# Performance work log

Measured on AMD Instinct MI355X. Metric: run time of the kernel, lower is better.

## Reference

```python
import jax, jax.numpy as jnp
import numpy as np

B, S, D = 2, 2048, 2048
H = 16
DR = 64      # qk_rope_head_dim
DN = 64      # qk_nope_head_dim
DQK = DN + DR
DV = 128     # v_head_dim
QLR = 1536   # q_lora_rank
KVLR = 1024  # kv_lora_rank
THETA = 10000.0


def setup_inputs() -> dict:
    key = jax.random.key(0)
    ks = jax.random.split(key, 8)
    init = lambda k, shape: (jax.random.normal(k, shape, jnp.float32) * 0.02)
    x = jax.random.normal(ks[0], (B, S, D), jnp.float32)
    wq_a = init(ks[1], (QLR, D))
    q_norm_w = jnp.ones((QLR,), jnp.float32)
    wq_b = init(ks[2], (H * DQK, QLR))
    wkv_a = init(ks[3], (KVLR + DR, D))
    kv_norm_w = jnp.ones((KVLR,), jnp.float32)
    wkv_b = init(ks[4], (H * (DN + DV), KVLR))
    wo = init(ks[5], (D, H * DV))
    # rotary frequencies: angle[t, i] = t / theta^(2i/DR)  (complex freqs_cis = cos + i sin)
    inv_freq = 1.0 / (THETA ** (jnp.arange(0, DR, 2, dtype=jnp.float32) / DR))
    ang = jnp.arange(S, dtype=jnp.float32)[:, None] * inv_freq[None, :]  # [S, DR/2]
    freqs_cos, freqs_sin = jnp.cos(ang), jnp.sin(ang)
    # causal additive mask (large negative instead of -inf for grad safety)
    mask = jnp.where(jnp.triu(jnp.ones((S, S), bool), 1), -1e9, 0.0).astype(jnp.float32)
    return dict(x=x, wq_a=wq_a, q_norm_w=q_norm_w, wq_b=wq_b, wkv_a=wkv_a,
                kv_norm_w=kv_norm_w, wkv_b=wkv_b, wo=wo, mask=mask,
                freqs_cos=freqs_cos, freqs_sin=freqs_sin, start_pos=0)


def _rmsnorm(x, w, eps=1e-6):
    return x * jax.lax.rsqrt(jnp.mean(x * x, axis=-1, keepdims=True) + eps) * w


def _rope(x, cos, sin):
    # x: [B, S, h, d]; complex multiply on interleaved (even, odd) pairs
    x0, x1 = x[..., ::2], x[..., 1::2]
    c = cos[None, :, None, :]
    s = sin[None, :, None, :]
    return jnp.stack([x0 * c - x1 * s, x0 * s + x1 * c], axis=-1).reshape(x.shape)


def reference(x, wq_a, q_norm_w, wq_b, wkv_a, kv_norm_w, wkv_b, wo,
              mask, freqs_cos, freqs_sin, start_pos):
    # start_pos == 0 prefill: KV cache[:end_pos] equals current K/V.
    scale = DQK ** -0.5
    # low-rank Q: wq_b(q_norm(wq_a(x)))
    q = _rmsnorm(x @ wq_a.T, q_norm_w) @ wq_b.T
    q = q.reshape(B, S, H, DQK)
    q_nope, q_pe = q[..., :DN], q[..., DN:]
    q_pe = _rope(q_pe, freqs_cos, freqs_sin)
    # latent KV
    kv = x @ wkv_a.T                              # [B, S, KVLR + DR]
    c_kv, k_pe = kv[..., :KVLR], kv[..., KVLR:]
    k_pe = _rope(k_pe[:, :, None, :], freqs_cos, freqs_sin)   # [B, S, 1, DR]
    kv2 = (_rmsnorm(c_kv, kv_norm_w) @ wkv_b.T).reshape(B, S, H, DN + DV)
    k_nope, v = kv2[..., :DN], kv2[..., DN:]
    k = jnp.concatenate([k_nope, jnp.broadcast_to(k_pe, (B, S, H, DR))], axis=-1)
    qf = jnp.concatenate([q_nope, q_pe], axis=-1)             # [B, S, H, DQK]
    # scores laid out [B, S(q), H, T(k)] as in the torch code
    scores = jnp.einsum('bshd,bthd->bsht', qf, k) * scale + mask[None, :, None, :]
    attn = jax.nn.softmax(scores.astype(jnp.float32), axis=-1).astype(x.dtype)
    out = jnp.einsum('bsht,bthd->bshd', attn, v)              # [B, S, H, DV]
    return out.reshape(B, S, H * DV) @ wo.T
```

## Files before the change

### kernel.cpp

```cpp
#include <hip/hip_runtime.h>
#include <hip/hip_bf16.h>


using bf16 = __hip_bfloat16;
typedef __attribute__((ext_vector_type(8))) short bf16x8;
typedef __attribute__((ext_vector_type(4))) float f32x4;

#define S_ 2048
#define NEG_BIG (-1e30f)
#define LOG2E 1.4426950408889634f

static __device__ __forceinline__ f32x4 mfma16(bf16x8 a, bf16x8 b, f32x4 c) {
    return __builtin_amdgcn_mfma_f32_16x16x32_bf16(a, b, c, 0, 0, 0);
}

static __device__ __forceinline__ void gload_lds16(const bf16* g, bf16* l) {
    __builtin_amdgcn_global_load_lds(
        (const __attribute__((address_space(1))) void*)g,
        (__attribute__((address_space(3))) void*)l, 16, 0, 0);
}

__global__ __launch_bounds__(256) void f2b(const float* __restrict__ src,
                                           bf16* __restrict__ dst, int n4) {
    int i = blockIdx.x * 256 + threadIdx.x;
    if (i < n4) {
        float4 v = ((const float4*)src)[i];
        alignas(8) bf16 t[4];
        t[0] = (bf16)v.x; t[1] = (bf16)v.y; t[2] = (bf16)v.z; t[3] = (bf16)v.w;
        ((uint2*)dst)[i] = *(const uint2*)t;
    }
}

template <bool C_F32>
__global__ __launch_bounds__(256) void gemm_bt(const bf16* __restrict__ A,
                                               const bf16* __restrict__ Bw,
                                               void* __restrict__ Cv,
                                               int M, int N, int K,
                                               int lda, int ldb, int ldc) {
    __shared__ bf16 As[2][128 * 32];
    __shared__ bf16 Bs[2][128 * 32];
    const int tid = threadIdx.x;
    int bx = blockIdx.x, by = blockIdx.y;
    {
        int nwg = gridDim.x * gridDim.y;
        if ((nwg & 7) == 0) {
            int wg = by * gridDim.x + bx;
            int swz = (wg & 7) * (nwg >> 3) + (wg >> 3);
            bx = swz % gridDim.x;
            by = swz / gridDim.x;
        }
    }
    const int m0 = bx * 128;
    const int n0 = by * 128;
    const int w = tid >> 6, lane = tid & 63, quad = lane >> 4, l15 = lane & 15;
    const int wr = (w >> 1) * 64, wc = (w & 1) * 64;

    f32x4 acc[4][4];
#pragma unroll
    for (int i = 0; i < 4; i++)
#pragma unroll
        for (int j = 0; j < 4; j++) acc[i][j] = (f32x4){0.f, 0.f, 0.f, 0.f};

    auto stage = [&](int buf, int k0) {
#pragma unroll
        for (int cc = 0; cc < 2; cc++) {
            int c = tid + cc * 256;
            int row = c >> 2;
            int chunk = (c & 3) ^ ((row >> 1) & 3);
            gload_lds16(A + (size_t)(m0 + row) * lda + k0 + chunk * 8, &As[buf][c * 8]);
            gload_lds16(Bw + (size_t)(n0 + row) * ldb + k0 + chunk * 8, &Bs[buf][c * 8]);
        }
    };

    stage(0, 0);
    __syncthreads();
    int cur = 0;
    for (int k0 = 0; k0 < K; k0 += 32) {
        if (k0 + 32 < K) stage(cur ^ 1, k0 + 32);
        const bf16* Asc = As[cur];
        const bf16* Bsc = Bs[cur];
        bf16x8 af[4], bfr[4];
#pragma unroll
        for (int mi = 0; mi < 4; mi++) {
            int row = wr + mi * 16 + l15;
            int chunkE = quad ^ ((row >> 1) & 3);
            af[mi] = *(const bf16x8*)(&Asc[row * 32 + chunkE * 8]);
        }
#pragma unroll
        for (int ni = 0; ni < 4; ni++) {
            int row = wc + ni * 16 + l15;
            int chunkE = quad ^ ((row >> 1) & 3);
            bfr[ni] = *(const bf16x8*)(&Bsc[row * 32 + chunkE * 8]);
        }
#pragma unroll
        for (int mi = 0; mi < 4; mi++)
#pragma unroll
            for (int ni = 0; ni < 4; ni++)
                acc[mi][ni] = mfma16(af[mi], bfr[ni], acc[mi][ni]);
        __syncthreads();
        cur ^= 1;
    }

#pragma unroll
    for (int mi = 0; mi < 4; mi++) {
#pragma unroll
        for (int ni = 0; ni < 4; ni++) {
            int col = n0 + wc + ni * 16 + l15;
            if (col < N) {
#pragma unroll
                for (int r = 0; r < 4; r++) {
                    int row = m0 + wr + mi * 16 + quad * 4 + r;
                    if (C_F32) ((float*)Cv)[(size_t)row * ldc + col] = acc[mi][ni][r];
                    else       ((bf16*)Cv)[(size_t)row * ldc + col] = (bf16)acc[mi][ni][r];
                }
            }
        }
    }
}

__global__ void rmsnorm_ip(bf16* __restrict__ buf, const float* __restrict__ w,
                           int cols, int ld) {
    int row = blockIdx.x;
    bf16* p = buf + (size_t)row * ld;
    float ss = 0.f;
    for (int c = threadIdx.x; c < cols; c += 256) {
        float v = __bfloat162float(p[c]);
        ss += v * v;
    }
#pragma unroll
    for (int off = 32; off; off >>= 1) ss += __shfl_down(ss, off, 64);
    __shared__ float red[4];
    __shared__ float rnorm_s;
    if ((threadIdx.x & 63) == 0) red[threadIdx.x >> 6] = ss;
    __syncthreads();
    if (threadIdx.x == 0)
        rnorm_s = rsqrtf((red[0] + red[1] + red[2] + red[3]) / cols + 1e-6f);
    __syncthreads();
    float rn = rnorm_s;
    for (int c = threadIdx.x; c < cols; c += 256) {
        float v = __bfloat162float(p[c]);
        p[c] = (bf16)(v * rn * w[c]);
    }
}

__global__ void rope_k(const bf16* __restrict__ cq, bf16* __restrict__ kpe,
                       const float* __restrict__ fc, const float* __restrict__ fs) {
    int id = blockIdx.x * 256 + threadIdx.x;
    int row = id >> 5, i = id & 31;
    int s = row & (S_ - 1);
    const bf16* p = cq + (size_t)row * 2624 + 1024 + 2 * i;
    float x0 = __bfloat162float(p[0]), x1 = __bfloat162float(p[1]);
    float c = fc[s * 32 + i], sn = fs[s * 32 + i];
    bf16* q = kpe + (size_t)row * 64 + 2 * i;
    q[0] = (bf16)(x0 * c - x1 * sn);
    q[1] = (bf16)(x0 * sn + x1 * c);
}

__global__ void rope_q(bf16* __restrict__ qb, const float* __restrict__ fc,
                       const float* __restrict__ fs) {
    int id = blockIdx.x * 256 + threadIdx.x;
    int row = id >> 9, rest = id & 511, h = rest >> 5, i = rest & 31;
    int s = row & (S_ - 1);
    bf16* p = qb + (size_t)row * 2048 + h * 128 + 64 + 2 * i;
    float x0 = __bfloat162float(p[0]), x1 = __bfloat162float(p[1]);
    float c = fc[s * 32 + i], sn = fs[s * 32 + i];
    p[0] = (bf16)(x0 * c - x1 * sn);
    p[1] = (bf16)(x0 * sn + x1 * c);
}

__global__ __launch_bounds__(512) void attn_kernel(const bf16* __restrict__ Qg,
                                                   const bf16* __restrict__ KV2,
                                                   const bf16* __restrict__ KPE,
                                                   bf16* __restrict__ Og) {
    __shared__ bf16 Ks[64 * 128];
    __shared__ bf16 Vt[128 * 64];
    const int tid = threadIdx.x;
    const int h = blockIdx.y;
    const int b = blockIdx.z;
    const int w = tid >> 6, lane = tid & 63, quad = lane >> 4, l15 = lane & 15;
    const int grp = w >> 2, wl = w & 3;
    const int jB = 31 - (int)blockIdx.x;
    const int q0 = (grp ? jB : (int)blockIdx.x) * 64;
    const int qrow = q0 + wl * 16 + l15;
    const float scl2 = 0.08838834764831845f * LOG2E;

    bf16x8 qf[4];
    {
        const bf16* qp = Qg + ((size_t)(b * S_) + qrow) * 2048 + h * 128 + quad * 8;
#pragma unroll
        for (int kk = 0; kk < 4; kk++) qf[kk] = *(const bf16x8*)(qp + kk * 32);
    }

    f32x4 acc_o[8];
#pragma unroll
    for (int j = 0; j < 8; j++) acc_o[j] = (f32x4){0.f, 0.f, 0.f, 0.f};
    float m_i = NEG_BIG, l_i = 0.f;
    const int s_base = q0 + wl * 16 + quad * 4;
    const int tend = jB * 64;

    const int dv0 = (tid >> 4) * 4;
    const int tv0 = (tid & 15) * 4;

    for (int t0 = 0; t0 <= tend; t0 += 64) {
        __syncthreads();
#pragma unroll
        for (int cc = 0; cc < 2; cc++) {
            int c = tid + cc * 512;
            int trow = c >> 4, chunk = c & 15;
            int col8 = chunk * 8;
            size_t grow = (size_t)(b * S_) + t0 + trow;
            int4 v;
            if (col8 < 64) v = *(const int4*)(KV2 + grow * 3072 + h * 192 + col8);
            else           v = *(const int4*)(KPE + grow * 64 + col8 - 64);
            int chunkE = chunk ^ (trow & 7);
            *(int4*)(&Ks[trow * 128 + chunkE * 8]) = v;
        }
        {
            size_t grow0 = (size_t)(b * S_) + t0 + tv0;
            alignas(16) bf16 va[4][4];
#pragma unroll
            for (int i = 0; i < 4; i++)
                *(uint2*)va[i] = *(const uint2*)(KV2 + (grow0 + i) * 3072 + h * 192 + 64 + dv0);
#pragma unroll
            for (int j = 0; j < 4; j++) {
                alignas(8) bf16 tmp[4] = {va[0][j], va[1][j], va[2][j], va[3][j]};
                int dv = dv0 + j;
                int cE = (tv0 >> 3) ^ (dv & 7);
                *(uint2*)(&Vt[dv * 64 + cE * 8 + (tv0 & 7)]) = *(uint2*)tmp;
            }
        }
        __syncthreads();
        if (t0 > q0) continue;

        f32x4 sc[4];
#pragma unroll
        for (int ni = 0; ni < 4; ni++) sc[ni] = (f32x4){0.f, 0.f, 0.f, 0.f};
#pragma unroll
        for (int kk = 0; kk < 4; kk++) {
#pragma unroll
            for (int ni = 0; ni < 4; ni++) {
                int trow = ni * 16 + l15;
                int chunkE = (kk * 4 + quad) ^ (trow & 7);
                bf16x8 kf = *(const bf16x8*)(&Ks[trow * 128 + chunkE * 8]);
                sc[ni] = mfma16(kf, qf[kk], sc[ni]);
            }
        }
        float xv[4][4];
        float pmax = NEG_BIG;
#pragma unroll
        for (int ni = 0; ni < 4; ni++) {
#pragma unroll
            for (int r = 0; r < 4; r++) {
                int t = t0 + ni * 16 + quad * 4 + r;
                float x = sc[ni][r] * scl2;
                if (t > qrow) x = NEG_BIG;
                xv[ni][r] = x;
                pmax = fmaxf(pmax, x);
            }
        }
        pmax = fmaxf(pmax, __shfl_xor(pmax, 16, 64));
        pmax = fmaxf(pmax, __shfl_xor(pmax, 32, 64));
        if (!__all(pmax - m_i <= 8.0f)) {
            float mn = fmaxf(m_i, pmax);
            float alpha = exp2f(m_i - mn);
            m_i = mn;
            l_i *= alpha;
            float ar[4];
#pragma unroll
            for (int r = 0; r < 4; r++) ar[r] = __shfl(alpha, quad * 4 + r, 64);
#pragma unroll
            for (int nj = 0; nj < 8; nj++)
#pragma unroll
                for (int r = 0; r < 4; r++) acc_o[nj][r] *= ar[r];
        }
        float rsum = 0.f;
#pragma unroll
        for (int ni = 0; ni < 4; ni++)
#pragma unroll
            for (int r = 0; r < 4; r++) {
                float e = exp2f(xv[ni][r] - m_i);
                xv[ni][r] = e;
                rsum += e;
            }
        rsum += __shfl_xor(rsum, 16, 64);
        rsum += __shfl_xor(rsum, 32, 64);
        l_i += rsum;

#pragma unroll
        for (int sg = 0; sg < 2; sg++) {
            alignas(16) bf16 pfa[8];
#pragma unroll
            for (int j = 0; j < 4; j++) {
                pfa[j]     = (bf16)xv[2 * sg][j];
                pfa[j + 4] = (bf16)xv[2 * sg + 1][j];
            }
            bf16x8 pf = *(const bf16x8*)pfa;
            const int cLo = sg * 4 + (quad >> 1);
            const int cHi = cLo + 2;
            const int off = (quad & 1) * 4;
#pragma unroll
            for (int nj = 0; nj < 8; nj++) {
                int dv = nj * 16 + l15;
                int d7 = dv & 7;
                alignas(16) bf16 vfa[8];
                *(uint2*)&vfa[0] = *(const uint2*)&Vt[dv * 64 + ((cLo ^ d7) * 8) + off];
                *(uint2*)&vfa[4] = *(const uint2*)&Vt[dv * 64 + ((cHi ^ d7) * 8) + off];
                bf16x8 vf = *(const bf16x8*)vfa;
                acc_o[nj] = mfma16(pf, vf, acc_o[nj]);
            }
        }
    }
    float lr[4];
#pragma unroll
    for (int r = 0; r < 4; r++) lr[r] = __shfl(l_i, quad * 4 + r, 64);
#pragma unroll
    for (int nj = 0; nj < 8; nj++) {
        int col = h * 128 + nj * 16 + l15;
#pragma unroll
        for (int r = 0; r < 4; r++) {
            float v = acc_o[nj][r] / lr[r];
            Og[((size_t)(b * S_) + s_base + r) * 2048 + col] = (bf16)v;
        }
    }
}

extern "C" void kernel_launch(void* const* d_in, const int* in_sizes, int n_in,
                              void* d_out, int out_size, void* d_ws, size_t ws_size,
                              hipStream_t stream) {
    const float* x        = (const float*)d_in[0];
    const float* wq_a     = (const float*)d_in[1];
    const float* q_norm_w = (const float*)d_in[2];
    const float* wq_b     = (const float*)d_in[3];
    const float* wkv_a    = (const float*)d_in[4];
    const float* kv_norm_w= (const float*)d_in[5];
    const float* wkv_b    = (const float*)d_in[6];
    const float* wo       = (const float*)d_in[7];
    const float* fcos     = (const float*)d_in[9];
    const float* fsin     = (const float*)d_in[10];
    float* out = (float*)d_out;

    char* ws = (char*)d_ws;
    bf16* kv2   = (bf16*)(ws);
    bf16* kpe   = (bf16*)(ws + 25165824);
    bf16* cq    = (bf16*)(ws + 25690112);
    bf16* xb    = (bf16*)(ws + 47185920);
    bf16* wslot = (bf16*)(ws + 63963136);
    bf16* attno = cq;
    bf16* qbuf  = (bf16*)d_out;

    dim3 blk(256);
    f2b<<<8192, blk, 0, stream>>>(x, xb, 2097152);
    f2b<<<2176, blk, 0, stream>>>(wkv_a, wslot, 557056);
    f2b<<<3072, blk, 0, stream>>>(wq_a, wslot + 1088 * 2048, 786432);
    gemm_bt<false><<<dim3(32, 21), blk, 0, stream>>>(xb, wslot, cq, 4096, 2624, 2048, 2048, 2048, 2624);
    rope_k<<<512, blk, 0, stream>>>(cq, kpe, fcos, fsin);
    rmsnorm_ip<<<4096, blk, 0, stream>>>(cq, kv_norm_w, 1024, 2624);
    f2b<<<3072, blk, 0, stream>>>(wkv_b, wslot, 786432);
    gemm_bt<false><<<dim3(32, 24), blk, 0, stream>>>(cq, wslot, kv2, 4096, 3072, 1024, 2624, 1024, 3072);
    rmsnorm_ip<<<4096, blk, 0, stream>>>(cq + 1088, q_norm_w, 1536, 2624);
    f2b<<<3072, blk, 0, stream>>>(wq_b, wslot, 786432);
    gemm_bt<false><<<dim3(32, 16), blk, 0, stream>>>(cq + 1088, wslot, qbuf, 4096, 2048, 1536, 2624, 1536, 2048);
    rope_q<<<8192, blk, 0, stream>>>(qbuf, fcos, fsin);
    attn_kernel<<<dim3(16, 16, 2), dim3(512), 0, stream>>>(qbuf, kv2, kpe, attno);
    f2b<<<4096, blk, 0, stream>>>(wo, wslot, 1048576);
    gemm_bt<true><<<dim3(32, 16), blk, 0, stream>>>(attno, wslot, out, 4096, 2048, 2048, 2048, 2048, 2048);
}
```

Measured before the change: 482.0 us.

## Split attention KV range into two halves with a separate combine kernel

The causal attention kernel now runs twice as many blocks. Each block covers either the lower or upper half of the key tiles for its paired query tiles and writes unnormalized-then-normalized partial outputs plus per-row (max, sum) statistics. A new combine kernel rescales and merges the two partial outputs before the output projection, aiming to raise parallelism and CU occupancy. This costs extra global traffic for the partial buffers and one more launch. Separately, the GEMM drops its workgroup index swizzle, which may change L2 reuse.

```diff
diff --git a/kernel.cpp b/kernel.cpp
--- a/kernel.cpp
+++ b/kernel.cpp
@@ -40,18 +40,8 @@
     __shared__ bf16 As[2][128 * 32];
     __shared__ bf16 Bs[2][128 * 32];
     const int tid = threadIdx.x;
-    int bx = blockIdx.x, by = blockIdx.y;
-    {
-        int nwg = gridDim.x * gridDim.y;
-        if ((nwg & 7) == 0) {
-            int wg = by * gridDim.x + bx;
-            int swz = (wg & 7) * (nwg >> 3) + (wg >> 3);
-            bx = swz % gridDim.x;
-            by = swz / gridDim.x;
-        }
-    }
-    const int m0 = bx * 128;
-    const int n0 = by * 128;
+    const int m0 = blockIdx.x * 128;
+    const int n0 = blockIdx.y * 128;
     const int w = tid >> 6, lane = tid & 63, quad = lane >> 4, l15 = lane & 15;
     const int wr = (w >> 1) * 64, wc = (w & 1) * 64;
 
@@ -171,12 +161,15 @@
 __global__ __launch_bounds__(512) void attn_kernel(const bf16* __restrict__ Qg,
                                                    const bf16* __restrict__ KV2,
                                                    const bf16* __restrict__ KPE,
-                                                   bf16* __restrict__ Og) {
+                                                   bf16* __restrict__ pO0,
+                                                   bf16* __restrict__ pO1,
+                                                   float2* __restrict__ ml) {
     __shared__ bf16 Ks[64 * 128];
     __shared__ bf16 Vt[128 * 64];
     const int tid = threadIdx.x;
     const int h = blockIdx.y;
-    const int b = blockIdx.z;
+    const int zz = blockIdx.z;
+    const int b = zz >> 1, half = zz & 1;
     const int w = tid >> 6, lane = tid & 63, quad = lane >> 4, l15 = lane & 15;
     const int grp = w >> 2, wl = w & 3;
     const int jB = 31 - (int)blockIdx.x;
@@ -184,6 +177,11 @@
     const int qrow = q0 + wl * 16 + l15;
     const float scl2 = 0.08838834764831845f * LOG2E;
 
+    const int nt = jB + 1;
+    const int h0 = (nt + 1) >> 1;
+    const int tlo = half ? h0 * 64 : 0;
+    const int thi = half ? (nt - 1) * 64 : (h0 - 1) * 64;
+
     bf16x8 qf[4];
     {
         const bf16* qp = Qg + ((size_t)(b * S_) + qrow) * 2048 + h * 128 + quad * 8;
@@ -196,12 +194,11 @@
     for (int j = 0; j < 8; j++) acc_o[j] = (f32x4){0.f, 0.f, 0.f, 0.f};
     float m_i = NEG_BIG, l_i = 0.f;
     const int s_base = q0 + wl * 16 + quad * 4;
-    const int tend = jB * 64;
 
     const int dv0 = (tid >> 4) * 4;
     const int tv0 = (tid & 15) * 4;
 
-    for (int t0 = 0; t0 <= tend; t0 += 64) {
+    for (int t0 = tlo; t0 <= thi; t0 += 64) {
         __syncthreads();
 #pragma unroll
         for (int cc = 0; cc < 2; cc++) {
@@ -313,15 +310,46 @@
     float lr[4];
 #pragma unroll
     for (int r = 0; r < 4; r++) lr[r] = __shfl(l_i, quad * 4 + r, 64);
+    bf16* pO = half ? pO1 : pO0;
 #pragma unroll
     for (int nj = 0; nj < 8; nj++) {
         int col = h * 128 + nj * 16 + l15;
 #pragma unroll
         for (int r = 0; r < 4; r++) {
-            float v = acc_o[nj][r] / lr[r];
-            Og[((size_t)(b * S_) + s_base + r) * 2048 + col] = (bf16)v;
-        }
-    }
+            float inv = lr[r] > 0.f ? 1.0f / lr[r] : 0.f;
+            float v = acc_o[nj][r] * inv;
+            pO[((size_t)(b * S_) + s_base + r) * 2048 + col] = (bf16)v;
+        }
+    }
+    if (quad == 0) ml[((size_t)zz * S_ + qrow) * 16 + h] = make_float2(m_i, l_i);
+}
+
+__global__ __launch_bounds__(256) void attn_combine(const bf16* __restrict__ pO0c,
+                                                    const bf16* __restrict__ pO1,
+                                                    const float2* __restrict__ ml,
+                                                    bf16* __restrict__ outb) {
+    int i = blockIdx.x * 256 + threadIdx.x;
+    int row = i >> 8;
+    int u = i & 255;
+    int col = u * 8;
+    int h = col >> 7;
+    int b = row >> 11, s = row & 2047;
+    float2 v0 = ml[((size_t)(b * 2 + 0) * S_ + s) * 16 + h];
+    float2 v1 = ml[((size_t)(b * 2 + 1) * S_ + s) * 16 + h];
+    float M = fmaxf(v0.x, v1.x);
+    float w0 = v0.y * exp2f(v0.x - M);
+    float w1 = v1.y * exp2f(v1.x - M);
+    float inv = 1.0f / (w0 + w1);
+    size_t base = (size_t)row * 2048 + col;
+    uint4 a = *(const uint4*)(pO0c + base);
+    uint4 c = *(const uint4*)(pO1 + base);
+    const bf16* pa = (const bf16*)&a;
+    const bf16* pc = (const bf16*)&c;
+    alignas(16) bf16 o[8];
+#pragma unroll
+    for (int j = 0; j < 8; j++)
+        o[j] = (bf16)((__bfloat162float(pa[j]) * w0 + __bfloat162float(pc[j]) * w1) * inv);
+    *(uint4*)(outb + base) = *(const uint4*)o;
 }
 
 extern "C" void kernel_launch(void* const* d_in, const int* in_sizes, int n_in,
@@ -345,6 +373,9 @@
     bf16* cq    = (bf16*)(ws + 25690112);
     bf16* xb    = (bf16*)(ws + 47185920);
     bf16* wslot = (bf16*)(ws + 63963136);
+    bf16* pO0   = cq;
+    float2* ml  = (float2*)(ws + 42467328);
+    bf16* pO1   = xb;
     bf16* attno = cq;
     bf16* qbuf  = (bf16*)d_out;
 
@@ -361,7 +392,8 @@
     f2b<<<3072, blk, 0, stream>>>(wq_b, wslot, 786432);
     gemm_bt<false><<<dim3(32, 16), blk, 0, stream>>>(cq + 1088, wslot, qbuf, 4096, 2048, 1536, 2624, 1536, 2048);
     rope_q<<<8192, blk, 0, stream>>>(qbuf, fcos, fsin);
-    attn_kernel<<<dim3(16, 16, 2), dim3(512), 0, stream>>>(qbuf, kv2, kpe, attno);
+    attn_kernel<<<dim3(16, 16, 4), dim3(512), 0, stream>>>(qbuf, kv2, kpe, pO0, pO1, ml);
+    attn_combine<<<8192, blk, 0, stream>>>(pO0, pO1, ml, attno);
     f2b<<<4096, blk, 0, stream>>>(wo, wslot, 1048576);
     gemm_bt<true><<<dim3(32, 16), blk, 0, stream>>>(attno, wslot, out, 4096, 2048, 2048, 2048, 2048, 2048);
 }
```

Result: slower. 534.4 us (+10.9%).

## Double-buffer attention K/V tiles with async global-to-LDS loads; drop GEMM swizzle

Applied to the files above, without the earlier changes.

The attention kernel now keeps two LDS buffers for K (split into nope and rope halves) and transposed V. The next tile is prefetched while the current one is computed, which removes one barrier per tile and overlaps load latency with MFMA work. K tiles are loaded with direct global-to-LDS loads instead of register round trips. The GEMM workgroup index swizzle is also removed, which may change L2 locality. In exchange, LDS use doubles, which may reduce occupancy.

```diff
diff --git a/kernel.cpp b/kernel.cpp
--- a/kernel.cpp
+++ b/kernel.cpp
@@ -40,18 +40,8 @@
     __shared__ bf16 As[2][128 * 32];
     __shared__ bf16 Bs[2][128 * 32];
     const int tid = threadIdx.x;
-    int bx = blockIdx.x, by = blockIdx.y;
-    {
-        int nwg = gridDim.x * gridDim.y;
-        if ((nwg & 7) == 0) {
-            int wg = by * gridDim.x + bx;
-            int swz = (wg & 7) * (nwg >> 3) + (wg >> 3);
-            bx = swz % gridDim.x;
-            by = swz / gridDim.x;
-        }
-    }
-    const int m0 = bx * 128;
-    const int n0 = by * 128;
+    const int m0 = blockIdx.x * 128;
+    const int n0 = blockIdx.y * 128;
     const int w = tid >> 6, lane = tid & 63, quad = lane >> 4, l15 = lane & 15;
     const int wr = (w >> 1) * 64, wc = (w & 1) * 64;
 
@@ -172,8 +162,9 @@
                                                    const bf16* __restrict__ KV2,
                                                    const bf16* __restrict__ KPE,
                                                    bf16* __restrict__ Og) {
-    __shared__ bf16 Ks[64 * 128];
-    __shared__ bf16 Vt[128 * 64];
+    __shared__ bf16 KnA[64 * 64], KpA[64 * 64];
+    __shared__ bf16 KnB[64 * 64], KpB[64 * 64];
+    __shared__ bf16 VtA[128 * 64], VtB[128 * 64];
     const int tid = threadIdx.x;
     const int h = blockIdx.y;
     const int b = blockIdx.z;
@@ -198,40 +189,31 @@
     const int s_base = q0 + wl * 16 + quad * 4;
     const int tend = jB * 64;
 
+    const int ktrow = tid >> 3, kc3 = tid & 7;
     const int dv0 = (tid >> 4) * 4;
     const int tv0 = (tid & 15) * 4;
 
-    for (int t0 = 0; t0 <= tend; t0 += 64) {
-        __syncthreads();
-#pragma unroll
-        for (int cc = 0; cc < 2; cc++) {
-            int c = tid + cc * 512;
-            int trow = c >> 4, chunk = c & 15;
-            int col8 = chunk * 8;
-            size_t grow = (size_t)(b * S_) + t0 + trow;
-            int4 v;
-            if (col8 < 64) v = *(const int4*)(KV2 + grow * 3072 + h * 192 + col8);
-            else           v = *(const int4*)(KPE + grow * 64 + col8 - 64);
-            int chunkE = chunk ^ (trow & 7);
-            *(int4*)(&Ks[trow * 128 + chunkE * 8]) = v;
-        }
-        {
-            size_t grow0 = (size_t)(b * S_) + t0 + tv0;
-            alignas(16) bf16 va[4][4];
-#pragma unroll
-            for (int i = 0; i < 4; i++)
-                *(uint2*)va[i] = *(const uint2*)(KV2 + (grow0 + i) * 3072 + h * 192 + 64 + dv0);
-#pragma unroll
-            for (int j = 0; j < 4; j++) {
-                alignas(8) bf16 tmp[4] = {va[0][j], va[1][j], va[2][j], va[3][j]};
-                int dv = dv0 + j;
-                int cE = (tv0 >> 3) ^ (dv & 7);
-                *(uint2*)(&Vt[dv * 64 + cE * 8 + (tv0 & 7)]) = *(uint2*)tmp;
-            }
-        }
-        __syncthreads();
-        if (t0 > q0) continue;
-
+    auto stageK = [&](bf16* Kn, bf16* Kp, int t0) {
+        size_t grow = (size_t)(b * S_) + t0 + ktrow;
+        int cs = (kc3 ^ (ktrow & 7)) * 8;
+        gload_lds16(KV2 + grow * 3072 + h * 192 + cs, Kn + tid * 8);
+        gload_lds16(KPE + grow * 64 + cs, Kp + tid * 8);
+    };
+    auto stageV = [&](bf16* Vt, int t0) {
+        size_t grow0 = (size_t)(b * S_) + t0 + tv0;
+        alignas(16) bf16 va[4][4];
+#pragma unroll
+        for (int i = 0; i < 4; i++)
+            *(uint2*)va[i] = *(const uint2*)(KV2 + (grow0 + i) * 3072 + h * 192 + 64 + dv0);
+#pragma unroll
+        for (int j = 0; j < 4; j++) {
+            alignas(8) bf16 tmp[4] = {va[0][j], va[1][j], va[2][j], va[3][j]};
+            int dv = dv0 + j;
+            int cE = (tv0 >> 3) ^ (dv & 7);
+            *(uint2*)(&Vt[dv * 64 + cE * 8 + (tv0 & 7)]) = *(uint2*)tmp;
+        }
+    };
+    auto compute = [&](const bf16* Kn, const bf16* Kp, const bf16* Vt, int t0) {
         f32x4 sc[4];
 #pragma unroll
         for (int ni = 0; ni < 4; ni++) sc[ni] = (f32x4){0.f, 0.f, 0.f, 0.f};
@@ -240,8 +222,14 @@
 #pragma unroll
             for (int ni = 0; ni < 4; ni++) {
                 int trow = ni * 16 + l15;
-                int chunkE = (kk * 4 + quad) ^ (trow & 7);
-                bf16x8 kf = *(const bf16x8*)(&Ks[trow * 128 + chunkE * 8]);
+                bf16x8 kf;
+                if (kk < 2) {
+                    int c3 = (kk * 4 + quad) ^ (trow & 7);
+                    kf = *(const bf16x8*)(&Kn[trow * 64 + c3 * 8]);
+                } else {
+                    int c3 = ((kk - 2) * 4 + quad) ^ (trow & 7);
+                    kf = *(const bf16x8*)(&Kp[trow * 64 + c3 * 8]);
+                }
                 sc[ni] = mfma16(kf, qf[kk], sc[ni]);
             }
         }
@@ -308,6 +296,21 @@
                 bf16x8 vf = *(const bf16x8*)vfa;
                 acc_o[nj] = mfma16(pf, vf, acc_o[nj]);
             }
+        }
+    };
+
+    stageK(KnA, KpA, 0);
+    stageV(VtA, 0);
+    __syncthreads();
+
+    for (int t0 = 0; t0 <= tend; t0 += 128) {
+        if (t0 + 64 <= tend) { stageK(KnB, KpB, t0 + 64); stageV(VtB, t0 + 64); }
+        if (t0 <= q0) compute(KnA, KpA, VtA, t0);
+        __syncthreads();
+        if (t0 + 64 <= tend) {
+            if (t0 + 128 <= tend) { stageK(KnA, KpA, t0 + 128); stageV(VtA, t0 + 128); }
+            if (t0 + 64 <= q0) compute(KnB, KpB, VtB, t0 + 64);
+            __syncthreads();
         }
     }
     float lr[4];
```

Result: no change. 480.5 us (-0.3%).
